# Kernel tuning notes

Hardware: AMD Instinct MI355X
Metric: run time of the kernel (lower is better)

The kernel has to match this reference:

```python
import jax, jax.numpy as jnp
import numpy as np

EPS = 1e-06

def knn(k_pos, q_pos, k):
    # k_pos: (B,N,3), q_pos: (B,S,3) -> idx (B,S,k) of nearest points in k_pos
    # squared euclidean distances (B,S,N)
    d2 = (jnp.sum(q_pos**2, -1)[:, :, None]
          - 2.0 * jnp.einsum('bsc,bnc->bsn', q_pos, k_pos)
          + jnp.sum(k_pos**2, -1)[:, None, :])
    _, idx = jax.lax.top_k(-d2, k)
    return idx

def linear(x, W, b):
    # torch nn.Linear: y = x @ W.T + b, W: (out,in)
    return jnp.einsum('...i,oi->...o', x, W) + b

def setup_inputs() -> dict:
    key = jax.random.key(0)
    ks = jax.random.split(key, 12)
    B, S, N, D = 4, 1024, 16384, 128
    sc = 1.0 / np.sqrt(D)
    inp = {
        'q_feat': jax.random.normal(ks[0], (B, S, D), jnp.float32),
        'k_feat': jax.random.normal(ks[1], (B, N, D), jnp.float32),
        'q_pos': jax.random.uniform(ks[2], (B, S, 3), jnp.float32),
        'k_pos': jax.random.uniform(ks[3], (B, N, 3), jnp.float32),
        'Wq': jax.random.normal(ks[4], (D, D), jnp.float32) * sc,
        'bq': jnp.zeros((D,), jnp.float32),
        'Wk': jax.random.normal(ks[5], (D, D), jnp.float32) * sc,
        'bk': jnp.zeros((D,), jnp.float32),
        'Wv': jax.random.normal(ks[6], (D, D), jnp.float32) * sc,
        'bv': jnp.zeros((D,), jnp.float32),
        'W1': jax.random.normal(ks[7], (D, 3), jnp.float32) * (1.0 / np.sqrt(3.0)),
        'b1': jnp.zeros((D,), jnp.float32),
        'W2': jax.random.normal(ks[8], (D, D), jnp.float32) * sc,
        'b2': jnp.zeros((D,), jnp.float32),
    }
    return inp

def reference(q_feat, k_feat, q_pos, k_pos, Wq, bq, Wk, bk, Wv, bv, W1, b1, W2, b2):
    KNN_K = 16
    q = linear(q_feat, Wq, bq)          # (B,S,D)
    k = linear(k_feat, Wk, bk)          # (B,N,D)
    v = linear(k_feat, Wv, bv)          # (B,N,D)
    idx = knn(k_pos, q_pos, KNN_K)      # (B,S,k)
    # gather neighbors: (B,S,k,D) and (B,S,k,3)
    k_nb = jnp.take_along_axis(k[:, None, :, :], idx[..., None], axis=2)
    v_nb = jnp.take_along_axis(v[:, None, :, :], idx[..., None], axis=2)
    kpos_nb = jnp.take_along_axis(k_pos[:, None, :, :], idx[..., None], axis=2)
    rel_pos = q_pos[:, :, None, :] - kpos_nb                     # (B,S,k,3)
    pe = linear(jax.nn.relu(linear(rel_pos, W1, b1)), W2, b2)    # (B,S,k,D)
    scores = jnp.sum(q[:, :, None, :] - k_nb + pe, axis=-1)      # (B,S,k)
    attn = jax.nn.softmax(scores, axis=-1)                       # softmax over k
    attn = attn / (jnp.sum(attn, axis=1, keepdims=True) + EPS)   # normalize over S
    out = jnp.sum(attn[..., None] * v_nb, axis=2)                # (B,S,D)
    return out
```

## Files before the change

### kernel.cpp

```cpp
#include <hip/hip_runtime.h>
#include <hip/hip_bf16.h>

#define BB 4
#define SS 1024
#define NPTS 16384
#define DD 128
#define EPSF 1e-6f

#define OFF_CQ     0
#define OFF_CK     128
#define OFF_W2S    256
#define OFF_SCL    384
#define OFF_COL    448
#define OFF_QSUM   512
#define OFF_KSUM   4608
#define OFF_IDX    70144
#define OFF_ATTN   135680
#define OFF_ASUM   201216
#define OFF_G      205312
#define OFF_WVT    729600

__device__ __forceinline__ unsigned long long shflxor_u64(unsigned long long v, int m) {
  unsigned int lo = (unsigned int)(v & 0xffffffffull);
  unsigned int hi = (unsigned int)(v >> 32);
  lo = (unsigned int)__shfl_xor((int)lo, m, 64);
  hi = (unsigned int)__shfl_xor((int)hi, m, 64);
  return ((unsigned long long)hi << 32) | (unsigned long long)lo;
}

__device__ __forceinline__ unsigned long long u64min(unsigned long long a, unsigned long long b) {
  return a < b ? a : b;
}

__device__ __forceinline__ unsigned long long wavemin_u64(unsigned long long v) {
#pragma unroll
  for (int m = 1; m <= 32; m <<= 1) v = u64min(v, shflxor_u64(v, m));
  return v;
}

__global__ __launch_bounds__(128) void k_prep(const float* __restrict__ Wq, const float* __restrict__ bq,
                       const float* __restrict__ Wk, const float* __restrict__ bk,
                       const float* __restrict__ Wv, const float* __restrict__ W2,
                       const float* __restrict__ b2, float* __restrict__ ws) {
  const int j = (int)blockIdx.x;
  const int t = threadIdx.x;
  __shared__ float pr[6];
  __shared__ float pb[6];
  float s0 = Wq[t * DD + j], s1 = Wk[t * DD + j], s2 = W2[t * DD + j];
#pragma unroll
  for (int m = 1; m <= 32; m <<= 1) {
    s0 += __shfl_xor(s0, m, 64);
    s1 += __shfl_xor(s1, m, 64);
    s2 += __shfl_xor(s2, m, 64);
  }
  if ((t & 63) == 0) { const int wv = t >> 6; pr[wv*3+0]=s0; pr[wv*3+1]=s1; pr[wv*3+2]=s2; }
  __syncthreads();
  if (t == 0) {
    ws[OFF_CQ + j]  = pr[0] + pr[3];
    ws[OFF_CK + j]  = pr[1] + pr[4];
    ws[OFF_W2S + j] = pr[2] + pr[5];
  }
  ws[OFF_WVT + j * DD + t] = Wv[t * DD + j];
  if (j == 1 && t < 64) ws[OFF_COL + t] = 0.f;
  if (j == 0) {
    float a0 = bq[t], a1 = bk[t], a2 = b2[t];
#pragma unroll
    for (int m = 1; m <= 32; m <<= 1) {
      a0 += __shfl_xor(a0, m, 64);
      a1 += __shfl_xor(a1, m, 64);
      a2 += __shfl_xor(a2, m, 64);
    }
    if ((t & 63) == 0) { const int wv = t >> 6; pb[wv*3+0]=a0; pb[wv*3+1]=a1; pb[wv*3+2]=a2; }
    __syncthreads();
    if (t == 0) {
      ws[OFF_SCL + 0] = pb[0] + pb[3];
      ws[OFF_SCL + 1] = pb[1] + pb[4];
      ws[OFF_SCL + 2] = pb[2] + pb[5];
    }
  }
}

__global__ __launch_bounds__(256) void k_rowsums(const float* __restrict__ kf,
                                                 const float* __restrict__ qf,
                                                 const float* __restrict__ kpos,
                                                 float* __restrict__ ws) {
  const int tid = threadIdx.x;
  const int pid = (int)blockIdx.x * 256 + tid;
  if (pid < BB * NPTS) {
    const float x = kpos[pid * 3 + 0], y = kpos[pid * 3 + 1], z = kpos[pid * 3 + 2];
    const float kk = __fadd_rn(__fadd_rn(__fmul_rn(x, x), __fmul_rn(y, y)), __fmul_rn(z, z));
    ((float4*)(ws + OFF_G))[pid] = make_float4(x, y, z, kk);
  }
  const int g = ((int)blockIdx.x * 256 + tid) >> 4;
  const int gl = tid & 15;
  const int ngroups = (int)gridDim.x * 16;
  const float bqs = ws[OFF_SCL + 0], bks = ws[OFF_SCL + 1];
  const int total = BB * NPTS + BB * SS;
  for (int row = g; row < total; row += ngroups) {
    const float* x;
    const float* c;
    if (row < BB * NPTS) { x = kf + (size_t)row * DD; c = ws + OFF_CK; }
    else                 { x = qf + (size_t)(row - BB * NPTS) * DD; c = ws + OFF_CQ; }
    float4 a  = *(const float4*)(x + gl * 4);
    float4 b  = *(const float4*)(x + 64 + gl * 4);
    float4 ca = *(const float4*)(c + gl * 4);
    float4 cb = *(const float4*)(c + 64 + gl * 4);
    float s = a.x * ca.x + a.y * ca.y + a.z * ca.z + a.w * ca.w
            + b.x * cb.x + b.y * cb.y + b.z * cb.z + b.w * cb.w;
    s += __shfl_xor(s, 1, 64);
    s += __shfl_xor(s, 2, 64);
    s += __shfl_xor(s, 4, 64);
    s += __shfl_xor(s, 8, 64);
    if (gl == 0) {
      if (row < BB * NPTS) ws[OFF_KSUM + row] = s + bks;
      else                 ws[OFF_QSUM + (row - BB * NPTS)] = s + bqs;
    }
  }
}

#define FORQ(X) X(0) X(1) X(2) X(3) X(4) X(5) X(6) X(7)

__global__ __launch_bounds__(512, 4) void k_knn(const float* __restrict__ qpos,
                                                const float* __restrict__ kpos,
                                                const float* __restrict__ W1,
                                                const float* __restrict__ b1,
                                                float* __restrict__ ws) {
  __shared__ unsigned long long cbuf[8][8][64];
  __shared__ float pmins[8][8][64];
  __shared__ int cnts[8][8];
  const int tid = threadIdx.x;
  const int w = tid >> 6, l = tid & 63;
  const int qbase = (int)blockIdx.x * 8;
  const int b = qbase >> 10;

  const float4* kp4 = (const float4*)(ws + OFF_G) + (size_t)b * NPTS;
  const float* kp = kpos + (size_t)b * NPTS * 3;

#define LOADQ(i) \
  const float qx##i = qpos[(size_t)(qbase + i) * 3 + 0]; \
  const float qy##i = qpos[(size_t)(qbase + i) * 3 + 1]; \
  const float qz##i = qpos[(size_t)(qbase + i) * 3 + 2]; \
  const float qq##i = __fadd_rn(__fadd_rn(__fmul_rn(qx##i, qx##i), __fmul_rn(qy##i, qy##i)), __fmul_rn(qz##i, qz##i));
  FORQ(LOADQ)
#undef LOADQ

  const int sbase = w * 2048;

#define DECLMN(i) float mn##i = 3.4e38f;
  FORQ(DECLMN)
#undef DECLMN
  {
    const float4* p0 = kp4 + sbase + l;
    float4 c0 = p0[0], c1 = p0[64], c2 = p0[128], c3 = p0[192];
    const float4* nx = p0 + 256;
#define P1Q(i, cc) { \
      const float dA = fmaf(qx##i, (cc).x, fmaf(qy##i, (cc).y, __fmul_rn(qz##i, (cc).z))); \
      const float d2a = __fadd_rn(fmaf(-2.0f, dA, qq##i), (cc).w); \
      mn##i = fminf(mn##i, d2a); }
#define P1_PT(cc, RELOAD) { \
      P1Q(0, cc) P1Q(1, cc) P1Q(2, cc) P1Q(3, cc) \
      P1Q(4, cc) P1Q(5, cc) P1Q(6, cc) P1Q(7, cc) \
      cc = RELOAD; }
    for (int t = 0; t < 8; ++t) {
      P1_PT(c0, nx[0])
      P1_PT(c1, nx[64])
      P1_PT(c2, nx[128])
      P1_PT(c3, nx[192])
      nx += 256;
    }
#undef P1_PT
  }
#define STMN(i) pmins[w][i][l] = mn##i;
  FORQ(STMN)
#undef STMN
  __syncthreads();

#define CUTQ(i) float cut##i; { \
    float m = pmins[0][i][l]; \
    m = fminf(m, pmins[1][i][l]); m = fminf(m, pmins[2][i][l]); \
    m = fminf(m, pmins[3][i][l]); m = fminf(m, pmins[4][i][l]); \
    m = fminf(m, pmins[5][i][l]); m = fminf(m, pmins[6][i][l]); \
    m = fminf(m, pmins[7][i][l]); \
    m = fminf(m, __shfl_xor(m, 16, 64)); \
    m = fminf(m, __shfl_xor(m, 32, 64)); \
    m = fmaxf(m, __shfl_xor(m, 1, 64)); \
    m = fmaxf(m, __shfl_xor(m, 2, 64)); \
    m = fmaxf(m, __shfl_xor(m, 4, 64)); \
    m = fmaxf(m, __shfl_xor(m, 8, 64)); \
    cut##i = m + 2e-5f; }
  FORQ(CUTQ)
#undef CUTQ

#define DECLCNT(i) int cnt##i = 0;
  FORQ(DECLCNT)
#undef DECLCNT
  {
    const float4* p0 = kp4 + sbase + l;
    float4 c0 = p0[0], c1 = p0[64], c2 = p0[128], c3 = p0[192];
    const float4* nx = p0 + 256;
    int p = sbase + l;
#define P2Q(i, cc, pp) { \
      const float dA = fmaf(qx##i, (cc).x, fmaf(qy##i, (cc).y, __fmul_rn(qz##i, (cc).z))); \
      const float d2a = __fadd_rn(fmaf(-2.0f, dA, qq##i), (cc).w); \
      const bool pred = (d2a <= cut##i); \
      const unsigned long long mask = __ballot(pred); \
      if (mask) { \
        if (pred) { \
          const float dotE = __fadd_rn(__fadd_rn(__fmul_rn(qz##i, (cc).z), __fmul_rn(qy##i, (cc).y)), __fmul_rn(qx##i, (cc).x)); \
          const float d2e = __fadd_rn(__fsub_rn(qq##i, __fmul_rn(2.0f, dotE)), (cc).w); \
          unsigned int u = __float_as_uint(d2e); \
          u ^= (unsigned int)((int)u >> 31) | 0x80000000u; \
          const int off = __builtin_amdgcn_mbcnt_hi((unsigned int)(mask >> 32), \
                          __builtin_amdgcn_mbcnt_lo((unsigned int)mask, 0)); \
          const int pos = cnt##i + off; \
          if (pos < 64) cbuf[i][w][pos] = ((unsigned long long)u << 32) | (unsigned int)(pp); \
        } \
        cnt##i += (int)__popcll(mask); \
      } }
#define P2_PT(cc, RELOAD, POFF) { \
      P2Q(0, cc, p + POFF) P2Q(1, cc, p + POFF) P2Q(2, cc, p + POFF) P2Q(3, cc, p + POFF) \
      P2Q(4, cc, p + POFF) P2Q(5, cc, p + POFF) P2Q(6, cc, p + POFF) P2Q(7, cc, p + POFF) \
      cc = RELOAD; }
    for (int t = 0; t < 8; ++t) {
      P2_PT(c0, nx[0], 0)
      P2_PT(c1, nx[64], 64)
      P2_PT(c2, nx[128], 128)
      P2_PT(c3, nx[192], 192)
      nx += 256;
      p += 256;
    }
#undef P2_PT
#undef P2Q
  }
#define STCNT(i) if (l == 0) cnts[i][w] = (cnt##i > 64 ? 64 : cnt##i);
  FORQ(STCNT)
#undef STCNT
  __syncthreads();

  const int qi = w;
  const int q = qbase + qi;
  unsigned long long cand[8];
#pragma unroll
  for (int i = 0; i < 8; ++i) {
    const int cn = cnts[qi][i];
    cand[i] = (l < cn) ? cbuf[qi][i][l] : ~0ull;
  }
  unsigned long long lmin = cand[0]; int lpos = 0;
#pragma unroll
  for (int i = 1; i < 8; ++i) { if (cand[i] < lmin) { lmin = cand[i]; lpos = i; } }
  unsigned long long sel64 = 0;
  for (int r = 0; r < 16; ++r) {
    const unsigned long long m = wavemin_u64(lmin);
    if (l == r) sel64 = m;
    if (lmin == m) {
#pragma unroll
      for (int i = 0; i < 8; ++i) cand[i] = (lpos == i) ? ~0ull : cand[i];
      lmin = cand[0]; lpos = 0;
#pragma unroll
      for (int i = 1; i < 8; ++i) { if (cand[i] < lmin) { lmin = cand[i]; lpos = i; } }
    }
  }
  const int myidx = (int)(sel64 & 0xffffffffull);
  if (l < 16) ((int*)(ws + OFF_IDX))[q * 16 + l] = myidx;

  const float* qpw = qpos + (size_t)q * 3;
  const float gx = qpw[0], gy = qpw[1], gz = qpw[2];
  const int j = l & 15;
  const int pj = __shfl(myidx, j, 64);
  const float* kpj = kp + (size_t)pj * 3;
  const float rx = gx - kpj[0];
  const float ry = gy - kpj[1];
  const float rz = gz - kpj[2];
  float pe = 0.f;
  const int i0 = (l >> 4) * 32;
  for (int i = i0; i < i0 + 32; ++i) {
    float hh = fmaf(rx, W1[i * 3 + 0], fmaf(ry, W1[i * 3 + 1], fmaf(rz, W1[i * 3 + 2], b1[i])));
    hh = fmaxf(hh, 0.f);
    pe = fmaf(hh, ws[OFF_W2S + i], pe);
  }
  pe += __shfl_xor(pe, 16, 64);
  pe += __shfl_xor(pe, 32, 64);
  float score = ws[OFF_QSUM + q] - ws[OFF_KSUM + b * NPTS + pj] + pe + ws[OFF_SCL + 2];
  float mx = score;
  mx = fmaxf(mx, __shfl_xor(mx, 1, 64));
  mx = fmaxf(mx, __shfl_xor(mx, 2, 64));
  mx = fmaxf(mx, __shfl_xor(mx, 4, 64));
  mx = fmaxf(mx, __shfl_xor(mx, 8, 64));
  const float e = expf(score - mx);
  float se = e;
  se += __shfl_xor(se, 1, 64);
  se += __shfl_xor(se, 2, 64);
  se += __shfl_xor(se, 4, 64);
  se += __shfl_xor(se, 8, 64);
  const float attn = e / se;
  if (l < 16) {
    ws[OFF_ATTN + q * 16 + l] = attn;
    atomicAdd(&ws[OFF_COL + b * 16 + l], attn);
  }
}

__global__ __launch_bounds__(256) void k_gather(const float* __restrict__ kf,
                                                float* __restrict__ ws) {
  const int tid = threadIdx.x;
  const int w = tid >> 6, l = tid & 63;
  const int q = (int)blockIdx.x * 4 + w;
  const int b = q >> 10;
  float a = 0.f;
  int pidx = 0;
  if (l < 16) {
    a = ws[OFF_ATTN + q * 16 + l] / (ws[OFF_COL + b * 16 + l] + EPSF);
    pidx = ((const int*)(ws + OFF_IDX))[q * 16 + l];
  }
  float asum = a;
  asum += __shfl_xor(asum, 1, 64);
  asum += __shfl_xor(asum, 2, 64);
  asum += __shfl_xor(asum, 4, 64);
  asum += __shfl_xor(asum, 8, 64);
  if (l == 0) ws[OFF_ASUM + q] = asum;
  const float* kb = kf + (size_t)b * NPTS * DD;
  float acc0 = 0.f, acc1 = 0.f;
#pragma unroll
  for (int jj = 0; jj < 16; ++jj) {
    const float aj = __shfl(a, jj, 64);
    const int pj = __shfl(pidx, jj, 64);
    const float* row = kb + (size_t)pj * DD;
    acc0 = fmaf(aj, row[l], acc0);
    acc1 = fmaf(aj, row[64 + l], acc1);
  }
  ws[OFF_G + (size_t)q * DD + l] = acc0;
  ws[OFF_G + (size_t)q * DD + 64 + l] = acc1;
}

__global__ __launch_bounds__(256) void k_out(const float* __restrict__ bv,
                                             const float* __restrict__ ws,
                                             float* __restrict__ out) {
  __shared__ float xg[16 * 128];
  __shared__ float as_s[16];
  const int tid = threadIdx.x;
  const int rbase = (int)blockIdx.x * 16;
  for (int e = tid; e < 16 * 128; e += 256) xg[e] = ws[OFF_G + (size_t)rbase * DD + e];
  if (tid < 16) as_s[tid] = ws[OFF_ASUM + rbase + tid];
  __syncthreads();
  const int o = tid & 127, rg = tid >> 7;
  const float bvo = bv[o];
  float acc[8];
#pragma unroll
  for (int r = 0; r < 8; ++r) acc[r] = as_s[rg * 8 + r] * bvo;
  for (int i = 0; i < DD; ++i) {
    const float wv = ws[OFF_WVT + i * DD + o];
#pragma unroll
    for (int r = 0; r < 8; ++r) acc[r] = fmaf(wv, xg[(rg * 8 + r) * 128 + i], acc[r]);
  }
#pragma unroll
  for (int r = 0; r < 8; ++r) out[(size_t)(rbase + rg * 8 + r) * DD + o] = acc[r];
}

extern "C" void kernel_launch(void* const* d_in, const int* in_sizes, int n_in,
                              void* d_out, int out_size, void* d_ws, size_t ws_size,
                              hipStream_t stream) {
  const float* qf   = (const float*)d_in[0];
  const float* kf   = (const float*)d_in[1];
  const float* qpos = (const float*)d_in[2];
  const float* kpos = (const float*)d_in[3];
  const float* Wq   = (const float*)d_in[4];
  const float* bq   = (const float*)d_in[5];
  const float* Wk   = (const float*)d_in[6];
  const float* bk   = (const float*)d_in[7];
  const float* Wv   = (const float*)d_in[8];
  const float* bv   = (const float*)d_in[9];
  const float* W1   = (const float*)d_in[10];
  const float* b1   = (const float*)d_in[11];
  const float* W2   = (const float*)d_in[12];
  const float* b2   = (const float*)d_in[13];
  float* ws  = (float*)d_ws;
  float* out = (float*)d_out;

  k_prep<<<128, 128, 0, stream>>>(Wq, bq, Wk, bk, Wv, W2, b2, ws);
  k_rowsums<<<1024, 256, 0, stream>>>(kf, qf, kpos, ws);
  k_knn<<<512, 512, 0, stream>>>(qpos, kpos, W1, b1, ws);
  k_gather<<<1024, 256, 0, stream>>>(kf, ws);
  k_out<<<256, 256, 0, stream>>>(bv, ws, out);
}
```

Measured before the change: 182.3 us.

## Fuse prep into rowsums, fuse gather with output GEMV, remap knn blocks per XCD

Merges the weight-prep kernel into the row-sum kernel: every block recomputes the Wq/Wk column sums and bias sums into shared memory, so the separate launch and global round-trip go away. The gather kernel and the Wv output projection are fused so gathered rows stay in shared memory instead of passing through the workspace. The knn block index is remapped so blocks on the same XCD work on the same batch, aiming for better L2 locality. In exchange, each of the 1024 pre blocks redundantly reads 2×128×128 weights, and the fused output kernel uses 8 rows per block, giving less Wv reuse.

After: 173.1 us. 1.05x faster.

```diff
diff --git a/kernel.cpp b/kernel.cpp
--- a/kernel.cpp
+++ b/kernel.cpp
@@ -38,69 +38,90 @@
   return v;
 }
 
-__global__ __launch_bounds__(128) void k_prep(const float* __restrict__ Wq, const float* __restrict__ bq,
-                       const float* __restrict__ Wk, const float* __restrict__ bk,
-                       const float* __restrict__ Wv, const float* __restrict__ W2,
-                       const float* __restrict__ b2, float* __restrict__ ws) {
-  const int j = (int)blockIdx.x;
-  const int t = threadIdx.x;
-  __shared__ float pr[6];
-  __shared__ float pb[6];
-  float s0 = Wq[t * DD + j], s1 = Wk[t * DD + j], s2 = W2[t * DD + j];
-#pragma unroll
-  for (int m = 1; m <= 32; m <<= 1) {
-    s0 += __shfl_xor(s0, m, 64);
-    s1 += __shfl_xor(s1, m, 64);
-    s2 += __shfl_xor(s2, m, 64);
-  }
-  if ((t & 63) == 0) { const int wv = t >> 6; pr[wv*3+0]=s0; pr[wv*3+1]=s1; pr[wv*3+2]=s2; }
-  __syncthreads();
-  if (t == 0) {
-    ws[OFF_CQ + j]  = pr[0] + pr[3];
-    ws[OFF_CK + j]  = pr[1] + pr[4];
-    ws[OFF_W2S + j] = pr[2] + pr[5];
-  }
-  ws[OFF_WVT + j * DD + t] = Wv[t * DD + j];
-  if (j == 1 && t < 64) ws[OFF_COL + t] = 0.f;
-  if (j == 0) {
-    float a0 = bq[t], a1 = bk[t], a2 = b2[t];
+__global__ __launch_bounds__(256) void k_pre(const float* __restrict__ kf,
+                                             const float* __restrict__ qf,
+                                             const float* __restrict__ kpos,
+                                             const float* __restrict__ Wq,
+                                             const float* __restrict__ bq,
+                                             const float* __restrict__ Wk,
+                                             const float* __restrict__ bk,
+                                             const float* __restrict__ Wv,
+                                             const float* __restrict__ W2,
+                                             const float* __restrict__ b2,
+                                             float* __restrict__ ws) {
+  const int tid = threadIdx.x;
+  const int bid = (int)blockIdx.x;
+  __shared__ __align__(16) float cq_s[128];
+  __shared__ __align__(16) float ck_s[128];
+  __shared__ float part[256];
+  __shared__ float scl_s[2];
+
+  {
+    const int j = tid & 127, h = tid >> 7;
+    const int r0 = h * 64;
+    float sq = 0.f, sk = 0.f;
+    for (int r = r0; r < r0 + 64; ++r) {
+      sq += Wq[r * DD + j];
+      sk += Wk[r * DD + j];
+    }
+    part[tid] = sq;
+    __syncthreads();
+    if (h == 0) cq_s[j] = part[j] + part[128 + j];
+    __syncthreads();
+    part[tid] = sk;
+    __syncthreads();
+    if (h == 0) ck_s[j] = part[j] + part[128 + j];
+  }
+  if (tid < 64) {
+    float a0 = bq[tid] + bq[tid + 64];
+    float a1 = bk[tid] + bk[tid + 64];
 #pragma unroll
     for (int m = 1; m <= 32; m <<= 1) {
       a0 += __shfl_xor(a0, m, 64);
       a1 += __shfl_xor(a1, m, 64);
-      a2 += __shfl_xor(a2, m, 64);
-    }
-    if ((t & 63) == 0) { const int wv = t >> 6; pb[wv*3+0]=a0; pb[wv*3+1]=a1; pb[wv*3+2]=a2; }
+    }
+    if (tid == 0) { scl_s[0] = a0; scl_s[1] = a1; }
+  }
+
+  if (bid < 128) {
+    if (tid < 128) ws[OFF_WVT + bid * DD + tid] = Wv[tid * DD + bid];
+  } else if (bid == 128) {
+    if (tid < 64) ws[OFF_COL + tid] = 0.f;
+  } else if (bid == 256) {
+    const int j = tid & 127, h = tid >> 7;
+    const int r0 = h * 64;
+    float s2 = 0.f;
+    for (int r = r0; r < r0 + 64; ++r) s2 += W2[r * DD + j];
     __syncthreads();
-    if (t == 0) {
-      ws[OFF_SCL + 0] = pb[0] + pb[3];
-      ws[OFF_SCL + 1] = pb[1] + pb[4];
-      ws[OFF_SCL + 2] = pb[2] + pb[5];
-    }
-  }
-}
-
-__global__ __launch_bounds__(256) void k_rowsums(const float* __restrict__ kf,
-                                                 const float* __restrict__ qf,
-                                                 const float* __restrict__ kpos,
-                                                 float* __restrict__ ws) {
-  const int tid = threadIdx.x;
-  const int pid = (int)blockIdx.x * 256 + tid;
+    part[tid] = s2;
+    __syncthreads();
+    if (h == 0) ws[OFF_W2S + j] = part[j] + part[128 + j];
+    if (tid < 64) {
+      float a2 = b2[tid] + b2[tid + 64];
+#pragma unroll
+      for (int m = 1; m <= 32; m <<= 1) a2 += __shfl_xor(a2, m, 64);
+      if (tid == 0) ws[OFF_SCL + 2] = a2;
+    }
+  }
+
+  const int pid = bid * 256 + tid;
   if (pid < BB * NPTS) {
     const float x = kpos[pid * 3 + 0], y = kpos[pid * 3 + 1], z = kpos[pid * 3 + 2];
     const float kk = __fadd_rn(__fadd_rn(__fmul_rn(x, x), __fmul_rn(y, y)), __fmul_rn(z, z));
     ((float4*)(ws + OFF_G))[pid] = make_float4(x, y, z, kk);
   }
-  const int g = ((int)blockIdx.x * 256 + tid) >> 4;
+  __syncthreads();
+  const float bqs = scl_s[0], bks = scl_s[1];
+
+  const int g = (bid * 256 + tid) >> 4;
   const int gl = tid & 15;
   const int ngroups = (int)gridDim.x * 16;
-  const float bqs = ws[OFF_SCL + 0], bks = ws[OFF_SCL + 1];
   const int total = BB * NPTS + BB * SS;
   for (int row = g; row < total; row += ngroups) {
     const float* x;
     const float* c;
-    if (row < BB * NPTS) { x = kf + (size_t)row * DD; c = ws + OFF_CK; }
-    else                 { x = qf + (size_t)(row - BB * NPTS) * DD; c = ws + OFF_CQ; }
+    if (row < BB * NPTS) { x = kf + (size_t)row * DD; c = ck_s; }
+    else                 { x = qf + (size_t)(row - BB * NPTS) * DD; c = cq_s; }
     float4 a  = *(const float4*)(x + gl * 4);
     float4 b  = *(const float4*)(x + 64 + gl * 4);
     float4 ca = *(const float4*)(c + gl * 4);
@@ -130,8 +151,12 @@
   __shared__ int cnts[8][8];
   const int tid = threadIdx.x;
   const int w = tid >> 6, l = tid & 63;
-  const int qbase = (int)blockIdx.x * 8;
-  const int b = qbase >> 10;
+  const int bid = (int)blockIdx.x;
+  const int xcd = bid & 7, s = bid >> 3;
+  const int batch = xcd & 3;
+  const int idx = ((xcd >> 2) << 6) + s;
+  const int qbase = batch * 1024 + idx * 8;
+  const int b = batch;
 
   const float4* kp4 = (const float4*)(ws + OFF_G) + (size_t)b * NPTS;
   const float* kp = kpos + (size_t)b * NPTS * 3;
@@ -299,60 +324,60 @@
   }
 }
 
-__global__ __launch_bounds__(256) void k_gather(const float* __restrict__ kf,
-                                                float* __restrict__ ws) {
+__global__ __launch_bounds__(256) void k_go(const float* __restrict__ kf,
+                                            const float* __restrict__ bv,
+                                            const float* __restrict__ ws,
+                                            float* __restrict__ out) {
+  __shared__ float xg[8 * 128];
+  __shared__ float as_s[8];
   const int tid = threadIdx.x;
   const int w = tid >> 6, l = tid & 63;
-  const int q = (int)blockIdx.x * 4 + w;
-  const int b = q >> 10;
-  float a = 0.f;
-  int pidx = 0;
-  if (l < 16) {
-    a = ws[OFF_ATTN + q * 16 + l] / (ws[OFF_COL + b * 16 + l] + EPSF);
-    pidx = ((const int*)(ws + OFF_IDX))[q * 16 + l];
-  }
-  float asum = a;
-  asum += __shfl_xor(asum, 1, 64);
-  asum += __shfl_xor(asum, 2, 64);
-  asum += __shfl_xor(asum, 4, 64);
-  asum += __shfl_xor(asum, 8, 64);
-  if (l == 0) ws[OFF_ASUM + q] = asum;
+  const int qbase = (int)blockIdx.x * 8;
+  const int b = qbase >> 10;
   const float* kb = kf + (size_t)b * NPTS * DD;
-  float acc0 = 0.f, acc1 = 0.f;
-#pragma unroll
-  for (int jj = 0; jj < 16; ++jj) {
-    const float aj = __shfl(a, jj, 64);
-    const int pj = __shfl(pidx, jj, 64);
-    const float* row = kb + (size_t)pj * DD;
-    acc0 = fmaf(aj, row[l], acc0);
-    acc1 = fmaf(aj, row[64 + l], acc1);
-  }
-  ws[OFF_G + (size_t)q * DD + l] = acc0;
-  ws[OFF_G + (size_t)q * DD + 64 + l] = acc1;
-}
-
-__global__ __launch_bounds__(256) void k_out(const float* __restrict__ bv,
-                                             const float* __restrict__ ws,
-                                             float* __restrict__ out) {
-  __shared__ float xg[16 * 128];
-  __shared__ float as_s[16];
-  const int tid = threadIdx.x;
-  const int rbase = (int)blockIdx.x * 16;
-  for (int e = tid; e < 16 * 128; e += 256) xg[e] = ws[OFF_G + (size_t)rbase * DD + e];
-  if (tid < 16) as_s[tid] = ws[OFF_ASUM + rbase + tid];
+
+#pragma unroll
+  for (int u = 0; u < 2; ++u) {
+    const int qi = w * 2 + u;
+    const int q = qbase + qi;
+    float a = 0.f;
+    int pidx = 0;
+    if (l < 16) {
+      a = ws[OFF_ATTN + q * 16 + l] / (ws[OFF_COL + b * 16 + l] + EPSF);
+      pidx = ((const int*)(ws + OFF_IDX))[q * 16 + l];
+    }
+    float asum = a;
+    asum += __shfl_xor(asum, 1, 64);
+    asum += __shfl_xor(asum, 2, 64);
+    asum += __shfl_xor(asum, 4, 64);
+    asum += __shfl_xor(asum, 8, 64);
+    if (l == 0) as_s[qi] = asum;
+    float acc0 = 0.f, acc1 = 0.f;
+#pragma unroll
+    for (int jj = 0; jj < 16; ++jj) {
+      const float aj = __shfl(a, jj, 64);
+      const int pj = __shfl(pidx, jj, 64);
+      const float* row = kb + (size_t)pj * DD;
+      acc0 = fmaf(aj, row[l], acc0);
+      acc1 = fmaf(aj, row[64 + l], acc1);
+    }
+    xg[qi * 128 + l] = acc0;
+    xg[qi * 128 + 64 + l] = acc1;
+  }
   __syncthreads();
+
   const int o = tid & 127, rg = tid >> 7;
   const float bvo = bv[o];
-  float acc[8];
-#pragma unroll
-  for (int r = 0; r < 8; ++r) acc[r] = as_s[rg * 8 + r] * bvo;
+  float acc[4];
+#pragma unroll
+  for (int r = 0; r < 4; ++r) acc[r] = as_s[rg * 4 + r] * bvo;
   for (int i = 0; i < DD; ++i) {
     const float wv = ws[OFF_WVT + i * DD + o];
 #pragma unroll
-    for (int r = 0; r < 8; ++r) acc[r] = fmaf(wv, xg[(rg * 8 + r) * 128 + i], acc[r]);
-  }
-#pragma unroll
-  for (int r = 0; r < 8; ++r) out[(size_t)(rbase + rg * 8 + r) * DD + o] = acc[r];
+    for (int r = 0; r < 4; ++r) acc[r] = fmaf(wv, xg[(rg * 4 + r) * 128 + i], acc[r]);
+  }
+#pragma unroll
+  for (int r = 0; r < 4; ++r) out[(size_t)(qbase + rg * 4 + r) * DD + o] = acc[r];
 }
 
 extern "C" void kernel_launch(void* const* d_in, const int* in_sizes, int n_in,
@@ -375,9 +400,7 @@
   float* ws  = (float*)d_ws;
   float* out = (float*)d_out;
 
-  k_prep<<<128, 128, 0, stream>>>(Wq, bq, Wk, bk, Wv, W2, b2, ws);
-  k_rowsums<<<1024, 256, 0, stream>>>(kf, qf, kpos, ws);
+  k_pre<<<1024, 256, 0, stream>>>(kf, qf, kpos, Wq, bq, Wk, bk, Wv, W2, b2, ws);
   k_knn<<<512, 512, 0, stream>>>(qpos, kpos, W1, b1, ws);
-  k_gather<<<1024, 256, 0, stream>>>(kf, ws);
-  k_out<<<256, 256, 0, stream>>>(bv, ws, out);
-}
+  k_go<<<512, 256, 0, stream>>>(kf, bv, ws, out);
+}
```
